# Optimization experiments

Hardware: AMD Instinct MI355X
Metric: run time of the kernel (lower is better)

The kernel has to match this reference:

```python
import jax, jax.numpy as jnp
import numpy as np

NUM_GROUPS = 32
EPS = 1e-6
NUM_HEADS = 8
HEAD_DIM = 64


def group_norm(x, gamma, beta):
    # x: [B, C, H, W]
    B, C, H, W = x.shape
    xg = x.reshape(B, NUM_GROUPS, C // NUM_GROUPS, H, W)
    mean = xg.mean(axis=(2, 3, 4), keepdims=True)
    var = xg.var(axis=(2, 3, 4), keepdims=True)
    xn = ((xg - mean) * jax.lax.rsqrt(var + EPS)).reshape(B, C, H, W)
    return xn * gamma[None, :, None, None] + beta[None, :, None, None]


def setup_inputs() -> dict:
    key = jax.random.key(0)
    ks = jax.random.split(key, 4)
    B, C, H, W = 8, 512, 32, 32
    hid = NUM_HEADS * HEAD_DIM  # 512
    x = jax.random.normal(ks[0], (B, C, H, W), dtype=jnp.float32)
    gamma = jnp.ones((C,), dtype=jnp.float32)
    beta = jnp.zeros((C,), dtype=jnp.float32)
    w_in = jax.random.normal(ks[1], (3 * hid, C), dtype=jnp.float32) * (1.0 / np.sqrt(C))
    b_in = jnp.zeros((3 * hid,), dtype=jnp.float32)
    w_out = jax.random.normal(ks[2], (C, hid), dtype=jnp.float32) * (1.0 / np.sqrt(hid))
    b_out = jnp.zeros((C,), dtype=jnp.float32)
    return {"x": x, "gamma": gamma, "beta": beta, "w_in": w_in, "b_in": b_in,
            "w_out": w_out, "b_out": b_out}


def reference(x, gamma, beta, w_in, b_in, w_out, b_out):
    B, C, H, W = x.shape
    n, c = NUM_HEADS, HEAD_DIM
    skip = x
    h = group_norm(x, gamma, beta)
    # 1x1 conv proj_in: [B, 3*n*c, H, W]
    qkv = jnp.einsum('oc,bchw->bohw', w_in, h) + b_in[None, :, None, None]
    qkv = qkv.reshape(B, 3, n, c, H * W)
    q, k, v = qkv[:, 0], qkv[:, 1], qkv[:, 2]  # each [B, n, c, HW]
    scale = 1.0 / np.sqrt(c)
    logits = jnp.einsum('bncq,bnck->bnqk', q, k) * scale  # [B, n, HW, HW]
    w = jax.nn.softmax(logits, axis=-1)
    out = jnp.einsum('bnqk,bnck->bncq', w, v)  # [B, n, c, HW]
    out = out.reshape(B, n * c, H, W)
    out = jnp.einsum('oc,bchw->bohw', w_out, out) + b_out[None, :, None, None]
    return out + skip
```

## Files before the change

kernel.cpp:

```cpp
#include <hip/hip_runtime.h>
#include <hip/hip_bf16.h>

#define B_    8
#define C_    512
#define HW_   1024
#define NG    32
#define GCH   16
#define EPSV  1e-6f

typedef __attribute__((ext_vector_type(8))) short short8;
typedef __attribute__((ext_vector_type(4))) short short4v;
typedef __attribute__((ext_vector_type(4))) float floatx4;

static __device__ __forceinline__ short f2bs(float f) {
  return __builtin_bit_cast(short, __float2bfloat16(f));
}
static __device__ __forceinline__ short4v pack4(float a, float b, float c, float d) {
  return (short4v){f2bs(a), f2bs(b), f2bs(c), f2bs(d)};
}
static __device__ __forceinline__ unsigned pk2(float a, float b) {
  return (unsigned)(unsigned short)f2bs(a) |
         ((unsigned)(unsigned short)f2bs(b) << 16);
}
#define MFMA(a, b, c) __builtin_amdgcn_mfma_f32_16x16x32_bf16((a), (b), (c), 0, 0, 0)

static __device__ __forceinline__ void glds16(const short* g, short* l) {
  __builtin_amdgcn_global_load_lds(
      (const __attribute__((address_space(1))) void*)g,
      (__attribute__((address_space(3))) void*)l, 16, 0, 0);
}

__global__ __launch_bounds__(256) void gn_cast_fused(
    const float* __restrict__ x, const float* __restrict__ gamma,
    const float* __restrict__ beta, short* __restrict__ ht,
    const float* __restrict__ w_in, short* __restrict__ wbf1,
    const float* __restrict__ w_out, short* __restrict__ wbf2) {
  int blk = blockIdx.x;
  int t = threadIdx.x;

  if (blk >= 256) {
    int i = (blk - 256) * 256 + t;
    const float* s; short* d; int j;
    if (i < 196608) { s = w_in; d = wbf1; j = i; }
    else            { s = w_out; d = wbf2; j = i - 196608; }
    float4 v = reinterpret_cast<const float4*>(s)[j];
    reinterpret_cast<short4v*>(d)[j] = pack4(v.x, v.y, v.z, v.w);
    return;
  }

  int b = blk >> 5, g = blk & 31;
  const float* xp = x + ((size_t)(b * C_) + g * GCH) * HW_;

  __shared__ float Ls[16 * 65];
  __shared__ float rs_[4], rss_[4], st_[2];

  float s = 0.f, ss = 0.f;
  for (int i = 0; i < 16; i++) {
    float4 v = *reinterpret_cast<const float4*>(xp + (t + i * 256) * 4);
    s  += (v.x + v.y) + (v.z + v.w);
    ss += (v.x * v.x + v.y * v.y) + (v.z * v.z + v.w * v.w);
  }
  for (int o = 32; o > 0; o >>= 1) {
    s  += __shfl_down(s, o);
    ss += __shfl_down(ss, o);
  }
  int wid = t >> 6, lane = t & 63;
  if (lane == 0) { rs_[wid] = s; rss_[wid] = ss; }
  __syncthreads();
  if (t == 0) {
    float stot  = rs_[0] + rs_[1] + rs_[2] + rs_[3];
    float sstot = rss_[0] + rss_[1] + rss_[2] + rss_[3];
    float mean = stot / 16384.f;
    float var  = sstot / 16384.f - mean * mean;
    st_[0] = mean;
    st_[1] = rsqrtf(var + EPSV);
  }
  __syncthreads();

  int r = t >> 4, c4 = t & 15;
  int ch = g * GCH + r;
  float ga = gamma[ch] * st_[1];
  float be = beta[ch] - st_[0] * ga;
  int sq = t >> 2, cq = t & 3;

  for (int stile = 0; stile < 16; stile++) {
    int s0 = stile * 64;
    float4 v = *reinterpret_cast<const float4*>(xp + r * HW_ + s0 + c4 * 4);
    Ls[r * 65 + c4 * 4 + 0] = v.x * ga + be;
    Ls[r * 65 + c4 * 4 + 1] = v.y * ga + be;
    Ls[r * 65 + c4 * 4 + 2] = v.z * ga + be;
    Ls[r * 65 + c4 * 4 + 3] = v.w * ga + be;
    __syncthreads();
    float a0 = Ls[(cq * 4 + 0) * 65 + sq];
    float a1 = Ls[(cq * 4 + 1) * 65 + sq];
    float a2 = Ls[(cq * 4 + 2) * 65 + sq];
    float a3 = Ls[(cq * 4 + 3) * 65 + sq];
    *reinterpret_cast<short4v*>(
        ht + ((size_t)b * 1024 + s0 + sq) * 512 + g * GCH + cq * 4) =
        pack4(a0, a1, a2, a3);
    __syncthreads();
  }
}

__global__ __launch_bounds__(256) void gemm_qkv(
    const short* __restrict__ Wb, const short* __restrict__ ht,
    const float* __restrict__ bias,
    short* __restrict__ Qt, short* __restrict__ Kt, short* __restrict__ Vn) {
  __shared__ short As[2][4096];
  __shared__ short Bs[2][4096];
  int bx = blockIdx.x, by = blockIdx.y, bb = blockIdx.z;
  int m0 = by * 128, n0 = bx * 128;
  int t = threadIdx.x;
  int w = t >> 6, lane = t & 63, n16 = lane & 15, quad = lane >> 4;
  int wm = (w >> 1) * 64, wn = (w & 1) * 64;

  const short* Wa = Wb + (size_t)(m0 + (t >> 2)) * 512 + (t & 3) * 8;
  const short* Xa = ht + (size_t)bb * 1024 * 512 +
                    (size_t)(n0 + (t >> 2)) * 512 + (t & 3) * 8;

#define STAGE(buf, kk)                                                \
  do {                                                                \
    glds16(Wa + (kk), &As[buf][t * 8]);                               \
    glds16(Wa + 64 * 512 + (kk), &As[buf][2048 + t * 8]);             \
    glds16(Xa + (kk), &Bs[buf][t * 8]);                               \
    glds16(Xa + 64 * 512 + (kk), &Bs[buf][2048 + t * 8]);             \
  } while (0)

  floatx4 acc[4][4];
  for (int i = 0; i < 4; i++)
    for (int j = 0; j < 4; j++) acc[i][j] = (floatx4){0.f, 0.f, 0.f, 0.f};

  STAGE(0, 0);
#pragma unroll 1
  for (int ks = 0; ks < 16; ks++) {
    int cur = ks & 1;
    __syncthreads();
    if (ks < 15) STAGE(cur ^ 1, (ks + 1) * 32);
    short8 a[4], b[4];
    for (int im = 0; im < 4; im++)
      a[im] = *reinterpret_cast<const short8*>(
          &As[cur][(wm + im * 16 + n16) * 32 + quad * 8]);
    for (int in = 0; in < 4; in++)
      b[in] = *reinterpret_cast<const short8*>(
          &Bs[cur][(wn + in * 16 + n16) * 32 + quad * 8]);
    for (int im = 0; im < 4; im++)
      for (int in = 0; in < 4; in++)
        acc[im][in] = MFMA(a[im], b[in], acc[im][in]);
  }
#undef STAGE

  if (m0 < 1024) {
    const bool isQ = (m0 < 512);
    short* base = isQ ? Qt : Kt;
    const float sc = isQ ? 0.125f : 1.0f;
    for (int im = 0; im < 4; im++) {
      int m = m0 + wm + im * 16 + quad * 4;
      int hh = (m >> 6) & 7, d0 = m & 63;
      float4 bi = *reinterpret_cast<const float4*>(&bias[m]);
      short* hb = base + (size_t)(bb * 8 + hh) * 1024 * 64 + d0;
      for (int in = 0; in < 4; in++) {
        int nn = n0 + wn + in * 16 + n16;
        *reinterpret_cast<short4v*>(hb + (size_t)nn * 64) =
            pack4((acc[im][in][0] + bi.x) * sc, (acc[im][in][1] + bi.y) * sc,
                  (acc[im][in][2] + bi.z) * sc, (acc[im][in][3] + bi.w) * sc);
      }
    }
  } else {
    for (int im = 0; im < 4; im++) {
      int m = m0 + wm + im * 16 + quad * 4;
      float4 bi = *reinterpret_cast<const float4*>(&bias[m]);
      int ch = m - 1024;
      for (int in = 0; in < 4; in++) {
        int nn = n0 + wn + in * 16 + n16;
        short* vp = Vn + (size_t)(bb * 512 + ch) * 1024 + nn;
        vp[0]    = f2bs(acc[im][in][0] + bi.x);
        vp[1024] = f2bs(acc[im][in][1] + bi.y);
        vp[2048] = f2bs(acc[im][in][2] + bi.z);
        vp[3072] = f2bs(acc[im][in][3] + bi.w);
      }
    }
  }
}

__global__ __launch_bounds__(256) void attn_mfma(
    const short* __restrict__ Qt, const short* __restrict__ Kt,
    const short* __restrict__ Vn, short* __restrict__ attnT) {
  int blk0 = blockIdx.x;
  int blk = (blk0 & 7) * 64 + (blk0 >> 3);
  int qb = blk & 7, h = (blk >> 3) & 7, b = blk >> 6;
  int t = threadIdx.x;
  int w = t >> 6, lane = t & 63, n16 = lane & 15, quad = lane >> 4;
  int q0 = qb * 128 + w * 32;
  int qhi = quad >> 1;
  int srcA = ((quad & 1) << 5) + n16;
  int srcB = srcA + 16;

  const short* Qp = Qt + (size_t)(b * 8 + h) * 1024 * 64;
  const short* Kp = Kt + (size_t)(b * 8 + h) * 1024 * 64;
  const short* Vp = Vn + (size_t)(b * 512 + h * 64) * 1024;

  short8 qa[2][2];
  for (int qt = 0; qt < 2; qt++)
    for (int f = 0; f < 2; f++)
      qa[qt][f] = *reinterpret_cast<const short8*>(
          Qp + (size_t)(q0 + qt * 16 + n16) * 64 + f * 32 + quad * 8);

  floatx4 O[2][4];
  float l[2] = {0.f, 0.f};
  for (int qt = 0; qt < 2; qt++)
    for (int i = 0; i < 4; i++) O[qt][i] = (floatx4){0.f, 0.f, 0.f, 0.f};

#define LOADK(dst, ktv)                                                      \
  do {                                                                       \
    int k0_ = (ktv) * 64;                                                    \
    for (int nt_ = 0; nt_ < 4; nt_++)                                        \
      for (int f_ = 0; f_ < 2; f_++)                                         \
        dst[nt_][f_] = *reinterpret_cast<const short8*>(                     \
            Kp + (size_t)(k0_ + nt_ * 16 + n16) * 64 + f_ * 32 + quad * 8);  \
  } while (0)

#define BODY(kf, ktv)                                                        \
  do {                                                                       \
    int k0_ = (ktv) * 64;                                                    \
    short8 v_[4][2];                                                         \
    for (int nd_ = 0; nd_ < 4; nd_++) {                                      \
      const short* vs_ =                                                     \
          Vp + (size_t)(nd_ * 16 + n16) * 1024 + k0_ + quad * 8;             \
      v_[nd_][0] = *reinterpret_cast<const short8*>(vs_);                    \
      v_[nd_][1] = *reinterpret_cast<const short8*>(vs_ + 32);               \
    }                                                                        \
    _Pragma("unroll")                                                        \
    for (int qt_ = 0; qt_ < 2; qt_++) {                                      \
      floatx4 T_[4];                                                         \
      _Pragma("unroll")                                                      \
      for (int nt_ = 0; nt_ < 4; nt_++) {                                    \
        floatx4 s_ = (floatx4){0.f, 0.f, 0.f, 0.f};                          \
        s_ = MFMA(kf[nt_][0], qa[qt_][0], s_);                               \
        T_[nt_] = MFMA(kf[nt_][1], qa[qt_][1], s_);                          \
      }                                                                      \
      unsigned u_[4][2];                                                     \
      _Pragma("unroll")                                                      \
      for (int nt_ = 0; nt_ < 4; nt_++) {                                    \
        float p0_ = __expf(T_[nt_][0]);                                      \
        float p1_ = __expf(T_[nt_][1]);                                      \
        float p2_ = __expf(T_[nt_][2]);                                      \
        float p3_ = __expf(T_[nt_][3]);                                      \
        l[qt_] += (p0_ + p1_) + (p2_ + p3_);                                 \
        u_[nt_][0] = pk2(p0_, p1_);                                         \
        u_[nt_][1] = pk2(p2_, p3_);                                         \
      }                                                                      \
      short8 pa_[2];                                                         \
      _Pragma("unroll")                                                      \
      for (int f_ = 0; f_ < 2; f_++) {                                       \
        unsigned a0_ = (unsigned)__shfl((int)u_[2 * f_ + 0][0], srcA);       \
        unsigned a1_ = (unsigned)__shfl((int)u_[2 * f_ + 1][0], srcA);       \
        unsigned b0_ = (unsigned)__shfl((int)u_[2 * f_ + 0][1], srcA);       \
        unsigned b1_ = (unsigned)__shfl((int)u_[2 * f_ + 1][1], srcA);       \
        unsigned c0_ = (unsigned)__shfl((int)u_[2 * f_ + 0][0], srcB);       \
        unsigned c1_ = (unsigned)__shfl((int)u_[2 * f_ + 1][0], srcB);       \
        unsigned d0_ = (unsigned)__shfl((int)u_[2 * f_ + 0][1], srcB);       \
        unsigned d1_ = (unsigned)__shfl((int)u_[2 * f_ + 1][1], srcB);       \
        uint4 wv_;                                                           \
        wv_.x = qhi ? a1_ : a0_;                                             \
        wv_.y = qhi ? b1_ : b0_;                                             \
        wv_.z = qhi ? c1_ : c0_;                                             \
        wv_.w = qhi ? d1_ : d0_;                                             \
        pa_[f_] = __builtin_bit_cast(short8, wv_);                           \
      }                                                                      \
      __builtin_amdgcn_s_setprio(1);                                         \
      _Pragma("unroll")                                                      \
      for (int nd_ = 0; nd_ < 4; nd_++) {                                    \
        O[qt_][nd_] = MFMA(pa_[0], v_[nd_][0], O[qt_][nd_]);                 \
        O[qt_][nd_] = MFMA(pa_[1], v_[nd_][1], O[qt_][nd_]);                 \
      }                                                                      \
      __builtin_amdgcn_s_setprio(0);                                         \
    }                                                                        \
  } while (0)

  short8 kfA[4][2], kfB[4][2];
  LOADK(kfA, 0);
#pragma unroll 1
  for (int kt = 0; kt < 16; kt += 2) {
    LOADK(kfB, kt + 1);
    BODY(kfA, kt);
    if (kt + 2 < 16) LOADK(kfA, kt + 2);
    BODY(kfB, kt + 1);
  }
#undef LOADK
#undef BODY

  for (int qt = 0; qt < 2; qt++) {
    float s = l[qt];
    s += __shfl_xor(s, 16);
    s += __shfl_xor(s, 32);
    for (int nd = 0; nd < 4; nd++)
      for (int r = 0; r < 4; r++) {
        float linv = 1.0f / __shfl(s, quad * 4 + r);
        int q = q0 + qt * 16 + quad * 4 + r;
        int ch = h * 64 + nd * 16 + n16;
        attnT[((size_t)b * 1024 + q) * 512 + ch] = f2bs(O[qt][nd][r] * linv);
      }
  }
}

__global__ __launch_bounds__(256) void gemm_out(
    const short* __restrict__ Wb, const short* __restrict__ Xt,
    const float* __restrict__ bias, const float* __restrict__ resid,
    float* __restrict__ out) {
  __shared__ short As[2][2048];
  __shared__ short Bs[2][2048];
  int bx = blockIdx.x, by = blockIdx.y, bb = blockIdx.z;
  int m0 = by * 64, n0 = bx * 64;
  int t = threadIdx.x;
  int w = t >> 6, lane = t & 63, n16 = lane & 15, quad = lane >> 4;
  int wm = (w >> 1) * 32, wn = (w & 1) * 32;

  const short* Wa = Wb + (size_t)(m0 + (t >> 2)) * 512 + (t & 3) * 8;
  const short* Xa = Xt + (size_t)bb * 1024 * 512 +
                    (size_t)(n0 + (t >> 2)) * 512 + (t & 3) * 8;

#define STAGE(buf, kk)                                                \
  do {                                                                \
    glds16(Wa + (kk), &As[buf][t * 8]);                               \
    glds16(Xa + (kk), &Bs[buf][t * 8]);                               \
  } while (0)

  floatx4 acc[2][2];
  for (int i = 0; i < 2; i++)
    for (int j = 0; j < 2; j++) acc[i][j] = (floatx4){0.f, 0.f, 0.f, 0.f};

  STAGE(0, 0);
#pragma unroll 1
  for (int ks = 0; ks < 16; ks++) {
    int cur = ks & 1;
    __syncthreads();
    if (ks < 15) STAGE(cur ^ 1, (ks + 1) * 32);
    short8 a[2], b[2];
    for (int im = 0; im < 2; im++)
      a[im] = *reinterpret_cast<const short8*>(
          &As[cur][(wm + im * 16 + n16) * 32 + quad * 8]);
    for (int in = 0; in < 2; in++)
      b[in] = *reinterpret_cast<const short8*>(
          &Bs[cur][(wn + in * 16 + n16) * 32 + quad * 8]);
    for (int im = 0; im < 2; im++)
      for (int in = 0; in < 2; in++)
        acc[im][in] = MFMA(a[im], b[in], acc[im][in]);
  }
#undef STAGE

  for (int im = 0; im < 2; im++) {
    int m = m0 + wm + im * 16 + quad * 4;
    float4 bi = *reinterpret_cast<const float4*>(&bias[m]);
    for (int in = 0; in < 2; in++) {
      int nn = n0 + wn + in * 16 + n16;
      size_t idx = ((size_t)bb * 512 + m) * 1024 + nn;
      out[idx]        = acc[im][in][0] + bi.x + resid[idx];
      out[idx + 1024] = acc[im][in][1] + bi.y + resid[idx + 1024];
      out[idx + 2048] = acc[im][in][2] + bi.z + resid[idx + 2048];
      out[idx + 3072] = acc[im][in][3] + bi.w + resid[idx + 3072];
    }
  }
}

extern "C" void kernel_launch(void* const* d_in, const int* in_sizes, int n_in,
                              void* d_out, int out_size, void* d_ws, size_t ws_size,
                              hipStream_t stream) {
  const float* x     = (const float*)d_in[0];
  const float* gamma = (const float*)d_in[1];
  const float* beta  = (const float*)d_in[2];
  const float* w_in  = (const float*)d_in[3];
  const float* b_in  = (const float*)d_in[4];
  const float* w_out = (const float*)d_in[5];
  const float* b_out = (const float*)d_in[6];
  float* out = (float*)d_out;

  char* ws = (char*)d_ws;
  short* ht    = (short*)ws;
  short* Qt    = (short*)(ws + (8u  << 20));
  short* Kt    = (short*)(ws + (16u << 20));
  short* Vn    = (short*)(ws + (24u << 20));
  short* attnT = (short*)(ws + (32u << 20));
  short* wbf1  = (short*)(ws + (40u << 20));
  short* wbf2  = (short*)(ws + (42u << 20));

  gn_cast_fused<<<1280, 256, 0, stream>>>(x, gamma, beta, ht,
                                          w_in, wbf1, w_out, wbf2);
  gemm_qkv<<<dim3(8, 12, B_), 256, 0, stream>>>(wbf1, ht, b_in, Qt, Kt, Vn);
  attn_mfma<<<512, 256, 0, stream>>>(Qt, Kt, Vn, attnT);
  gemm_out<<<dim3(16, 8, B_), 256, 0, stream>>>(wbf2, attnT, b_out, x, out);
}
```

Baseline: 188.2 us.

## Widen attention key tiles to 128, drop K double buffer, batch groupnorm transposes

The attention kernel now processes 128 keys per iteration instead of two 64-key tiles with explicit K register double-buffering. It computes all P fragments for both query tiles before loading V in halves, and a waves_per_eu(2) hint lets the compiler use more registers. The groupnorm-transpose kernel stages four 64-column tiles in shared memory per barrier pair, cutting the barrier count by four. The tradeoffs are losing the explicit K prefetch overlap, higher register pressure, and more LDS per block in the norm kernel.

Result: no change. 184.6 us (-1.9%).

```diff
diff --git a/kernel.cpp b/kernel.cpp
--- a/kernel.cpp
+++ b/kernel.cpp
@@ -51,7 +51,7 @@
   int b = blk >> 5, g = blk & 31;
   const float* xp = x + ((size_t)(b * C_) + g * GCH) * HW_;
 
-  __shared__ float Ls[16 * 65];
+  __shared__ float Ls[4 * 1040];
   __shared__ float rs_[4], rss_[4], st_[2];
 
   float s = 0.f, ss = 0.f;
@@ -83,21 +83,28 @@
   float be = beta[ch] - st_[0] * ga;
   int sq = t >> 2, cq = t & 3;
 
-  for (int stile = 0; stile < 16; stile++) {
-    int s0 = stile * 64;
-    float4 v = *reinterpret_cast<const float4*>(xp + r * HW_ + s0 + c4 * 4);
-    Ls[r * 65 + c4 * 4 + 0] = v.x * ga + be;
-    Ls[r * 65 + c4 * 4 + 1] = v.y * ga + be;
-    Ls[r * 65 + c4 * 4 + 2] = v.z * ga + be;
-    Ls[r * 65 + c4 * 4 + 3] = v.w * ga + be;
+  for (int it = 0; it < 4; it++) {
+    for (int sub = 0; sub < 4; sub++) {
+      int s0 = (it * 4 + sub) * 64;
+      float4 v = *reinterpret_cast<const float4*>(xp + r * HW_ + s0 + c4 * 4);
+      float* L = Ls + sub * 1040;
+      L[r * 65 + c4 * 4 + 0] = v.x * ga + be;
+      L[r * 65 + c4 * 4 + 1] = v.y * ga + be;
+      L[r * 65 + c4 * 4 + 2] = v.z * ga + be;
+      L[r * 65 + c4 * 4 + 3] = v.w * ga + be;
+    }
     __syncthreads();
-    float a0 = Ls[(cq * 4 + 0) * 65 + sq];
-    float a1 = Ls[(cq * 4 + 1) * 65 + sq];
-    float a2 = Ls[(cq * 4 + 2) * 65 + sq];
-    float a3 = Ls[(cq * 4 + 3) * 65 + sq];
-    *reinterpret_cast<short4v*>(
-        ht + ((size_t)b * 1024 + s0 + sq) * 512 + g * GCH + cq * 4) =
-        pack4(a0, a1, a2, a3);
+    for (int sub = 0; sub < 4; sub++) {
+      int s0 = (it * 4 + sub) * 64;
+      const float* L = Ls + sub * 1040;
+      float a0 = L[(cq * 4 + 0) * 65 + sq];
+      float a1 = L[(cq * 4 + 1) * 65 + sq];
+      float a2 = L[(cq * 4 + 2) * 65 + sq];
+      float a3 = L[(cq * 4 + 3) * 65 + sq];
+      *reinterpret_cast<short4v*>(
+          ht + ((size_t)b * 1024 + s0 + sq) * 512 + g * GCH + cq * 4) =
+          pack4(a0, a1, a2, a3);
+    }
     __syncthreads();
   }
 }
@@ -182,7 +189,8 @@
   }
 }
 
-__global__ __launch_bounds__(256) void attn_mfma(
+__global__ __launch_bounds__(256)
+__attribute__((amdgpu_waves_per_eu(2))) void attn_mfma(
     const short* __restrict__ Qt, const short* __restrict__ Kt,
     const short* __restrict__ Vn, short* __restrict__ attnT) {
   int blk0 = blockIdx.x;
@@ -210,84 +218,79 @@
   for (int qt = 0; qt < 2; qt++)
     for (int i = 0; i < 4; i++) O[qt][i] = (floatx4){0.f, 0.f, 0.f, 0.f};
 
-#define LOADK(dst, ktv)                                                      \
-  do {                                                                       \
-    int k0_ = (ktv) * 64;                                                    \
-    for (int nt_ = 0; nt_ < 4; nt_++)                                        \
-      for (int f_ = 0; f_ < 2; f_++)                                         \
-        dst[nt_][f_] = *reinterpret_cast<const short8*>(                     \
-            Kp + (size_t)(k0_ + nt_ * 16 + n16) * 64 + f_ * 32 + quad * 8);  \
-  } while (0)
-
-#define BODY(kf, ktv)                                                        \
-  do {                                                                       \
-    int k0_ = (ktv) * 64;                                                    \
-    short8 v_[4][2];                                                         \
-    for (int nd_ = 0; nd_ < 4; nd_++) {                                      \
-      const short* vs_ =                                                     \
-          Vp + (size_t)(nd_ * 16 + n16) * 1024 + k0_ + quad * 8;             \
-      v_[nd_][0] = *reinterpret_cast<const short8*>(vs_);                    \
-      v_[nd_][1] = *reinterpret_cast<const short8*>(vs_ + 32);               \
-    }                                                                        \
-    _Pragma("unroll")                                                        \
-    for (int qt_ = 0; qt_ < 2; qt_++) {                                      \
-      floatx4 T_[4];                                                         \
-      _Pragma("unroll")                                                      \
-      for (int nt_ = 0; nt_ < 4; nt_++) {                                    \
-        floatx4 s_ = (floatx4){0.f, 0.f, 0.f, 0.f};                          \
-        s_ = MFMA(kf[nt_][0], qa[qt_][0], s_);                               \
-        T_[nt_] = MFMA(kf[nt_][1], qa[qt_][1], s_);                          \
-      }                                                                      \
-      unsigned u_[4][2];                                                     \
-      _Pragma("unroll")                                                      \
-      for (int nt_ = 0; nt_ < 4; nt_++) {                                    \
-        float p0_ = __expf(T_[nt_][0]);                                      \
-        float p1_ = __expf(T_[nt_][1]);                                      \
-        float p2_ = __expf(T_[nt_][2]);                                      \
-        float p3_ = __expf(T_[nt_][3]);                                      \
-        l[qt_] += (p0_ + p1_) + (p2_ + p3_);                                 \
-        u_[nt_][0] = pk2(p0_, p1_);                                         \
-        u_[nt_][1] = pk2(p2_, p3_);                                         \
-      }                                                                      \
-      short8 pa_[2];                                                         \
-      _Pragma("unroll")                                                      \
-      for (int f_ = 0; f_ < 2; f_++) {                                       \
-        unsigned a0_ = (unsigned)__shfl((int)u_[2 * f_ + 0][0], srcA);       \
-        unsigned a1_ = (unsigned)__shfl((int)u_[2 * f_ + 1][0], srcA);       \
-        unsigned b0_ = (unsigned)__shfl((int)u_[2 * f_ + 0][1], srcA);       \
-        unsigned b1_ = (unsigned)__shfl((int)u_[2 * f_ + 1][1], srcA);       \
-        unsigned c0_ = (unsigned)__shfl((int)u_[2 * f_ + 0][0], srcB);       \
-        unsigned c1_ = (unsigned)__shfl((int)u_[2 * f_ + 1][0], srcB);       \
-        unsigned d0_ = (unsigned)__shfl((int)u_[2 * f_ + 0][1], srcB);       \
-        unsigned d1_ = (unsigned)__shfl((int)u_[2 * f_ + 1][1], srcB);       \
-        uint4 wv_;                                                           \
-        wv_.x = qhi ? a1_ : a0_;                                             \
-        wv_.y = qhi ? b1_ : b0_;                                             \
-        wv_.z = qhi ? c1_ : c0_;                                             \
-        wv_.w = qhi ? d1_ : d0_;                                             \
-        pa_[f_] = __builtin_bit_cast(short8, wv_);                           \
-      }                                                                      \
-      __builtin_amdgcn_s_setprio(1);                                         \
-      _Pragma("unroll")                                                      \
-      for (int nd_ = 0; nd_ < 4; nd_++) {                                    \
-        O[qt_][nd_] = MFMA(pa_[0], v_[nd_][0], O[qt_][nd_]);                 \
-        O[qt_][nd_] = MFMA(pa_[1], v_[nd_][1], O[qt_][nd_]);                 \
-      }                                                                      \
-      __builtin_amdgcn_s_setprio(0);                                         \
-    }                                                                        \
-  } while (0)
-
-  short8 kfA[4][2], kfB[4][2];
-  LOADK(kfA, 0);
+  short8 kf[8][2];
+  short8 vv[4][2];
+
 #pragma unroll 1
-  for (int kt = 0; kt < 16; kt += 2) {
-    LOADK(kfB, kt + 1);
-    BODY(kfA, kt);
-    if (kt + 2 < 16) LOADK(kfA, kt + 2);
-    BODY(kfB, kt + 1);
-  }
-#undef LOADK
-#undef BODY
+  for (int kt = 0; kt < 8; kt++) {
+    int k0 = kt * 128;
+#pragma unroll
+    for (int nt = 0; nt < 8; nt++)
+#pragma unroll
+      for (int f = 0; f < 2; f++)
+        kf[nt][f] = *reinterpret_cast<const short8*>(
+            Kp + (size_t)(k0 + nt * 16 + n16) * 64 + f * 32 + quad * 8);
+
+    short8 pa[2][4];
+#pragma unroll
+    for (int qt = 0; qt < 2; qt++) {
+      floatx4 T[8];
+#pragma unroll
+      for (int nt = 0; nt < 8; nt++) {
+        floatx4 s_ = (floatx4){0.f, 0.f, 0.f, 0.f};
+        s_ = MFMA(kf[nt][0], qa[qt][0], s_);
+        T[nt] = MFMA(kf[nt][1], qa[qt][1], s_);
+      }
+      unsigned u[8][2];
+#pragma unroll
+      for (int nt = 0; nt < 8; nt++) {
+        float p0 = __expf(T[nt][0]);
+        float p1 = __expf(T[nt][1]);
+        float p2 = __expf(T[nt][2]);
+        float p3 = __expf(T[nt][3]);
+        l[qt] += (p0 + p1) + (p2 + p3);
+        u[nt][0] = pk2(p0, p1);
+        u[nt][1] = pk2(p2, p3);
+      }
+#pragma unroll
+      for (int fr = 0; fr < 4; fr++) {
+        unsigned a0 = (unsigned)__shfl((int)u[2 * fr + 0][0], srcA);
+        unsigned a1 = (unsigned)__shfl((int)u[2 * fr + 1][0], srcA);
+        unsigned b0 = (unsigned)__shfl((int)u[2 * fr + 0][1], srcA);
+        unsigned b1 = (unsigned)__shfl((int)u[2 * fr + 1][1], srcA);
+        unsigned c0 = (unsigned)__shfl((int)u[2 * fr + 0][0], srcB);
+        unsigned c1 = (unsigned)__shfl((int)u[2 * fr + 1][0], srcB);
+        unsigned d0 = (unsigned)__shfl((int)u[2 * fr + 0][1], srcB);
+        unsigned d1 = (unsigned)__shfl((int)u[2 * fr + 1][1], srcB);
+        uint4 wv;
+        wv.x = qhi ? a1 : a0;
+        wv.y = qhi ? b1 : b0;
+        wv.z = qhi ? c1 : c0;
+        wv.w = qhi ? d1 : d0;
+        pa[qt][fr] = __builtin_bit_cast(short8, wv);
+      }
+    }
+
+#pragma unroll
+    for (int half = 0; half < 2; half++) {
+#pragma unroll
+      for (int nd = 0; nd < 4; nd++) {
+        const short* vs = Vp + (size_t)(nd * 16 + n16) * 1024 + k0 +
+                          half * 64 + quad * 8;
+        vv[nd][0] = *reinterpret_cast<const short8*>(vs);
+        vv[nd][1] = *reinterpret_cast<const short8*>(vs + 32);
+      }
+      __builtin_amdgcn_s_setprio(1);
+#pragma unroll
+      for (int qt = 0; qt < 2; qt++)
+#pragma unroll
+        for (int nd = 0; nd < 4; nd++) {
+          O[qt][nd] = MFMA(pa[qt][2 * half + 0], vv[nd][0], O[qt][nd]);
+          O[qt][nd] = MFMA(pa[qt][2 * half + 1], vv[nd][1], O[qt][nd]);
+        }
+      __builtin_amdgcn_s_setprio(0);
+    }
+  }
 
   for (int qt = 0; qt < 2; qt++) {
     float s = l[qt];
```

## Stage attention K/V tiles in swizzled LDS via async copies; batch groupnorm transpose

Applied to the files above, without the earlier changes.

The attention kernel now stages each 64-key K and V tile into double-buffered, XOR-swizzled shared memory using direct global-to-LDS copies. All four waves then read their MFMA fragments from LDS, instead of each wave fetching K and V separately from global memory. This is meant to cut redundant global and L2 traffic and hide load latency, at the cost of a block-wide barrier every tile and extra LDS use. Separately, the groupnorm transpose now writes four 64-column subtiles per barrier pair, reducing the number of __syncthreads calls.

Result: faster. 161.1 us (-14.4%).

```diff
diff --git a/kernel.cpp b/kernel.cpp
--- a/kernel.cpp
+++ b/kernel.cpp
@@ -51,7 +51,7 @@
   int b = blk >> 5, g = blk & 31;
   const float* xp = x + ((size_t)(b * C_) + g * GCH) * HW_;
 
-  __shared__ float Ls[16 * 65];
+  __shared__ float Ls[4 * 1040];
   __shared__ float rs_[4], rss_[4], st_[2];
 
   float s = 0.f, ss = 0.f;
@@ -83,21 +83,28 @@
   float be = beta[ch] - st_[0] * ga;
   int sq = t >> 2, cq = t & 3;
 
-  for (int stile = 0; stile < 16; stile++) {
-    int s0 = stile * 64;
-    float4 v = *reinterpret_cast<const float4*>(xp + r * HW_ + s0 + c4 * 4);
-    Ls[r * 65 + c4 * 4 + 0] = v.x * ga + be;
-    Ls[r * 65 + c4 * 4 + 1] = v.y * ga + be;
-    Ls[r * 65 + c4 * 4 + 2] = v.z * ga + be;
-    Ls[r * 65 + c4 * 4 + 3] = v.w * ga + be;
+  for (int it = 0; it < 4; it++) {
+    for (int sub = 0; sub < 4; sub++) {
+      int s0 = (it * 4 + sub) * 64;
+      float4 v = *reinterpret_cast<const float4*>(xp + r * HW_ + s0 + c4 * 4);
+      float* L = Ls + sub * 1040;
+      L[r * 65 + c4 * 4 + 0] = v.x * ga + be;
+      L[r * 65 + c4 * 4 + 1] = v.y * ga + be;
+      L[r * 65 + c4 * 4 + 2] = v.z * ga + be;
+      L[r * 65 + c4 * 4 + 3] = v.w * ga + be;
+    }
     __syncthreads();
-    float a0 = Ls[(cq * 4 + 0) * 65 + sq];
-    float a1 = Ls[(cq * 4 + 1) * 65 + sq];
-    float a2 = Ls[(cq * 4 + 2) * 65 + sq];
-    float a3 = Ls[(cq * 4 + 3) * 65 + sq];
-    *reinterpret_cast<short4v*>(
-        ht + ((size_t)b * 1024 + s0 + sq) * 512 + g * GCH + cq * 4) =
-        pack4(a0, a1, a2, a3);
+    for (int sub = 0; sub < 4; sub++) {
+      int s0 = (it * 4 + sub) * 64;
+      const float* L = Ls + sub * 1040;
+      float a0 = L[(cq * 4 + 0) * 65 + sq];
+      float a1 = L[(cq * 4 + 1) * 65 + sq];
+      float a2 = L[(cq * 4 + 2) * 65 + sq];
+      float a3 = L[(cq * 4 + 3) * 65 + sq];
+      *reinterpret_cast<short4v*>(
+          ht + ((size_t)b * 1024 + s0 + sq) * 512 + g * GCH + cq * 4) =
+          pack4(a0, a1, a2, a3);
+    }
     __syncthreads();
   }
 }
@@ -185,6 +192,8 @@
 __global__ __launch_bounds__(256) void attn_mfma(
     const short* __restrict__ Qt, const short* __restrict__ Kt,
     const short* __restrict__ Vn, short* __restrict__ attnT) {
+  __shared__ short KT[2][4096];
+  __shared__ short VT[2][4096];
   int blk0 = blockIdx.x;
   int blk = (blk0 & 7) * 64 + (blk0 >> 3);
   int qb = blk & 7, h = (blk >> 3) & 7, b = blk >> 6;
@@ -210,33 +219,44 @@
   for (int qt = 0; qt < 2; qt++)
     for (int i = 0; i < 4; i++) O[qt][i] = (floatx4){0.f, 0.f, 0.f, 0.f};
 
-#define LOADK(dst, ktv)                                                      \
+  int p0 = t * 16, p1 = 4096 + t * 16;
+  int r0 = p0 >> 7, c0 = (p0 & 127) ^ ((r0 & 7) << 4);
+  int r1 = p1 >> 7, c1 = (p1 & 127) ^ ((r1 & 7) << 4);
+
+#define STAGEKV(buf, ktv)                                                    \
   do {                                                                       \
-    int k0_ = (ktv) * 64;                                                    \
+    const char* Kb_ = (const char*)Kp + (ktv) * 8192;                        \
+    const char* Vb_ = (const char*)Vp + (ktv) * 128;                         \
+    glds16((const short*)(Kb_ + r0 * 128 + c0), &KT[buf][p0 >> 1]);          \
+    glds16((const short*)(Kb_ + r1 * 128 + c1), &KT[buf][p1 >> 1]);          \
+    glds16((const short*)(Vb_ + (size_t)r0 * 2048 + c0), &VT[buf][p0 >> 1]); \
+    glds16((const short*)(Vb_ + (size_t)r1 * 2048 + c1), &VT[buf][p1 >> 1]); \
+  } while (0)
+
+#define LDSOFF(row, colb) ((row) * 128 + (((colb) ^ (((row) & 7) << 4))))
+
+#define BODY(cur)                                                            \
+  do {                                                                       \
+    short8 kf_[4][2], v_[4][2];                                              \
+    _Pragma("unroll")                                                        \
     for (int nt_ = 0; nt_ < 4; nt_++)                                        \
-      for (int f_ = 0; f_ < 2; f_++)                                         \
-        dst[nt_][f_] = *reinterpret_cast<const short8*>(                     \
-            Kp + (size_t)(k0_ + nt_ * 16 + n16) * 64 + f_ * 32 + quad * 8);  \
-  } while (0)
-
-#define BODY(kf, ktv)                                                        \
-  do {                                                                       \
-    int k0_ = (ktv) * 64;                                                    \
-    short8 v_[4][2];                                                         \
-    for (int nd_ = 0; nd_ < 4; nd_++) {                                      \
-      const short* vs_ =                                                     \
-          Vp + (size_t)(nd_ * 16 + n16) * 1024 + k0_ + quad * 8;             \
-      v_[nd_][0] = *reinterpret_cast<const short8*>(vs_);                    \
-      v_[nd_][1] = *reinterpret_cast<const short8*>(vs_ + 32);               \
-    }                                                                        \
+      _Pragma("unroll")                                                      \
+      for (int f_ = 0; f_ < 2; f_++) {                                       \
+        kf_[nt_][f_] = *reinterpret_cast<const short8*>(                     \
+            (const char*)&KT[cur][0] +                                       \
+            LDSOFF(nt_ * 16 + n16, f_ * 64 + quad * 16));                    \
+        v_[nt_][f_] = *reinterpret_cast<const short8*>(                      \
+            (const char*)&VT[cur][0] +                                       \
+            LDSOFF(nt_ * 16 + n16, f_ * 64 + quad * 16));                    \
+      }                                                                      \
     _Pragma("unroll")                                                        \
     for (int qt_ = 0; qt_ < 2; qt_++) {                                      \
       floatx4 T_[4];                                                         \
       _Pragma("unroll")                                                      \
       for (int nt_ = 0; nt_ < 4; nt_++) {                                    \
         floatx4 s_ = (floatx4){0.f, 0.f, 0.f, 0.f};                          \
-        s_ = MFMA(kf[nt_][0], qa[qt_][0], s_);                               \
-        T_[nt_] = MFMA(kf[nt_][1], qa[qt_][1], s_);                          \
+        s_ = MFMA(kf_[nt_][0], qa[qt_][0], s_);                              \
+        T_[nt_] = MFMA(kf_[nt_][1], qa[qt_][1], s_);                         \
       }                                                                      \
       unsigned u_[4][2];                                                     \
       _Pragma("unroll")                                                      \
@@ -246,8 +266,8 @@
         float p2_ = __expf(T_[nt_][2]);                                      \
         float p3_ = __expf(T_[nt_][3]);                                      \
         l[qt_] += (p0_ + p1_) + (p2_ + p3_);                                 \
-        u_[nt_][0] = pk2(p0_, p1_);                                         \
-        u_[nt_][1] = pk2(p2_, p3_);                                         \
+        u_[nt_][0] = pk2(p0_, p1_);                                          \
+        u_[nt_][1] = pk2(p2_, p3_);                                          \
       }                                                                      \
       short8 pa_[2];                                                         \
       _Pragma("unroll")                                                      \
@@ -277,16 +297,16 @@
     }                                                                        \
   } while (0)
 
-  short8 kfA[4][2], kfB[4][2];
-  LOADK(kfA, 0);
+  STAGEKV(0, 0);
 #pragma unroll 1
-  for (int kt = 0; kt < 16; kt += 2) {
-    LOADK(kfB, kt + 1);
-    BODY(kfA, kt);
-    if (kt + 2 < 16) LOADK(kfA, kt + 2);
-    BODY(kfB, kt + 1);
-  }
-#undef LOADK
+  for (int kt = 0; kt < 16; kt++) {
+    int cur = kt & 1;
+    __syncthreads();
+    if (kt < 15) STAGEKV(cur ^ 1, kt + 1);
+    BODY(cur);
+  }
+#undef STAGEKV
+#undef LDSOFF
 #undef BODY
 
   for (int qt = 0; qt < 2; qt++) {
```
